# Optimization experiments

Measured on AMD Instinct MI355X. Metric: run time of the kernel, lower is better.

The kernel has to match this reference:

```python
import jax, jax.numpy as jnp
import numpy as np

B, S, D, DK = 4, 2048, 1024, 1024


def setup_inputs() -> dict:
    key = jax.random.key(0)
    kx, kq, kk, kv = jax.random.split(key, 4)
    return {
        "x": jax.random.normal(kx, (B, S, D), dtype=jnp.float32),
        "WQ": jax.random.normal(kq, (D, DK), dtype=jnp.float32),
        "WK": jax.random.normal(kk, (D, DK), dtype=jnp.float32),
        "WV": jax.random.normal(kv, (D, DK), dtype=jnp.float32),
    }


def reference(x, WQ, WK, WV):
    # q,k,v: [B,S,DK]
    q = x @ WQ
    k = x @ WK
    v = x @ WV
    scale = 1.0 / np.sqrt(DK).astype(np.float32)
    scores = jnp.einsum("bqd,bkd->bqk", q, k) * scale  # [B,S,S]
    # NOTE: original uses nn.Softmax(dim=1) -> normalize over the QUERY axis (axis 1)
    attn = jax.nn.softmax(scores, axis=1)
    return jnp.einsum("bqk,bkd->bqd", attn, v)
```

## Files before the change

### kernel.cpp

```cpp
#include <hip/hip_runtime.h>

constexpr int Bc  = 4;
constexpr int Sc  = 2048;
constexpr int Dc  = 1024;
constexpr int DKc = 1024;
constexpr long BSc = (long)Bc * Sc;

typedef __attribute__((ext_vector_type(8))) __bf16 bf16x8;
typedef __attribute__((ext_vector_type(4))) float  floatx4;

__device__ inline __bf16 f2bf(float f) {
  unsigned u = __builtin_bit_cast(unsigned, f);
  u = (u + 0x7FFFu + ((u >> 16) & 1u)) >> 16;
  unsigned short s = (unsigned short)u;
  return __builtin_bit_cast(__bf16, s);
}
__device__ inline float bf2f(__bf16 h) {
  unsigned u = ((unsigned)__builtin_bit_cast(unsigned short, h)) << 16;
  return __builtin_bit_cast(float, u);
}

__device__ inline void stage16(const __bf16* g, __bf16* l) {
  __builtin_amdgcn_global_load_lds(
      (const __attribute__((address_space(1))) unsigned int*)g,
      (__attribute__((address_space(3))) unsigned int*)l, 16, 0, 0);
}

__device__ __forceinline__ void bar_raw() {
  asm volatile("" ::: "memory");
  __builtin_amdgcn_s_barrier();
  asm volatile("" ::: "memory");
}
template <int N>
__device__ __forceinline__ void vmwait() {
  asm volatile("s_waitcnt vmcnt(%0)" :: "n"(N));
  __builtin_amdgcn_sched_barrier(0);
}

__global__ __launch_bounds__(256) void prep(
    const float* __restrict__ x,  __bf16* __restrict__ xhi, __bf16* __restrict__ xlo,
    const float* __restrict__ wq, __bf16* __restrict__ qhi, __bf16* __restrict__ qlo,
    const float* __restrict__ wk, __bf16* __restrict__ khi, __bf16* __restrict__ klo,
    const float* __restrict__ wv, __bf16* __restrict__ vthi) {
  __shared__ float tile[32][33];
  long blk = blockIdx.x;
  if (blk >= 40960) {
    int t   = (int)(blk - 40960);
    int bx  = t & 31, by = t >> 5;
    int thx = threadIdx.x & 31, thy = threadIdx.x >> 5;
    int xI  = bx * 32 + thx, yI = by * 32 + thy;
#pragma unroll
    for (int j = 0; j < 32; j += 8)
      tile[thy + j][thx] = wv[(long)(yI + j) * DKc + xI];
    __syncthreads();
    int xO = by * 32 + thx, yO = bx * 32 + thy;
#pragma unroll
    for (int j = 0; j < 32; j += 8)
      vthi[(long)(yO + j) * Dc + xO] = f2bf(tile[thx][thy + j]);
    return;
  }
  const float* in; __bf16 *hi, *lo; long base;
  if (blk < 32768)      { in = x;  hi = xhi; lo = xlo; base = blk * 256; }
  else if (blk < 36864) { in = wq; hi = qhi; lo = qlo; base = (blk - 32768) * 256; }
  else                  { in = wk; hi = khi; lo = klo; base = (blk - 36864) * 256; }
  long i = base + threadIdx.x;
  float f = in[i];
  __bf16 h = f2bf(f);
  hi[i] = h;
  lo[i] = f2bf(f - bf2f(h));
}

enum { MODE_QK = 0, MODE_V = 1, MODE_S = 2, MODE_PV = 3 };
constexpr int VSTR = 136;

template <int MODE>
__device__ __forceinline__ void gemm_body(
    char* smem,
    const __bf16* __restrict__ Ahi, const __bf16* __restrict__ Alo,
    const __bf16* __restrict__ Bhi, const __bf16* __restrict__ Blo,
    float* __restrict__ Cf, __bf16* __restrict__ Chi, __bf16* __restrict__ Clo,
    float* __restrict__ Pmax, float* __restrict__ Psum,
    const float* __restrict__ Ffac, float scale) {
  constexpr bool SPLIT = (MODE == MODE_QK || MODE == MODE_S);
  constexpr int  K = (MODE == MODE_PV) ? Sc : Dc;
  constexpr int  N = (MODE == MODE_S) ? Sc : DKc;
  constexpr long aBatch = (MODE == MODE_S) ? (long)Sc * DKc
                        : (MODE == MODE_PV) ? (long)Sc * Sc : 0;
  constexpr long bBatch = (MODE == MODE_S) ? (long)Sc * DKc
                        : (MODE == MODE_PV) ? (long)DKc * Sc : 0;
  constexpr long cBatch = (MODE == MODE_S) ? (long)Sc * Sc
                        : (MODE == MODE_PV) ? (long)Sc * DKc : 0;
  __bf16* sAh = (__bf16*)smem;
  __bf16* sBh = sAh + 128 * 32;
  __bf16* sAl = sBh + 128 * 32;
  __bf16* sBl = sAl + 128 * 32;

  const int b    = blockIdx.z;
  const int wave = threadIdx.x >> 6;
  const int lane = threadIdx.x & 63;
  const int wm   = wave >> 1;
  const int wn   = wave & 1;
  const int m0   = blockIdx.y * 128;
  const int n0   = blockIdx.x * 128;

  const __bf16* Ab  = Ahi + (long)b * aBatch + (long)m0 * K;
  const __bf16* Bb  = Bhi + (long)b * bBatch + (long)n0 * K;
  const __bf16* Abl = SPLIT ? Alo + (long)b * aBatch + (long)m0 * K : nullptr;
  const __bf16* Bbl = SPLIT ? Blo + (long)b * bBatch + (long)n0 * K : nullptr;
  const float*  Fb  = (MODE == MODE_PV)
                    ? Ffac + ((long)b * 8 + (blockIdx.y >> 1)) * Sc : nullptr;

  const int sr   = lane >> 2;
  const int sc_  = lane & 3;
  const int scol = (sc_ ^ ((sr >> 1) & 3)) * 8;

  floatx4 acc[4][4];
  const floatx4 zero = {0.f, 0.f, 0.f, 0.f};
#pragma unroll
  for (int i = 0; i < 4; ++i)
#pragma unroll
    for (int j = 0; j < 4; ++j) acc[i][j] = zero;

  const int frow = lane & 15;
  const int pko = ((lane >> 4) ^ ((frow >> 1) & 3)) * 8;

#pragma unroll 1
  for (int k0 = 0; k0 < K; k0 += 32) {
    if constexpr (MODE == MODE_PV) {
#pragma unroll
      for (int i = 0; i < 2; ++i) {
        const int rb = wave * 32 + i * 16;
        stage16(Bb + (long)(rb + sr) * K + k0 + scol, sBh + rb * 32);
      }
      const int tr = threadIdx.x >> 2;
      const int pc = threadIdx.x & 3;
#pragma unroll
      for (int h = 0; h < 2; ++h) {
        int r  = h * 64 + tr;
        int lc = pc ^ ((r >> 1) & 3);
        bf16x8 pv = *(const bf16x8*)(Ab + (long)r * K + k0 + lc * 8);
        const float* fp = Fb + k0 + lc * 8;
        bf16x8 o;
#pragma unroll
        for (int j = 0; j < 8; ++j) o[j] = f2bf(bf2f(pv[j]) * fp[j]);
        *(bf16x8*)(sAh + r * 32 + pc * 8) = o;
      }
    } else {
#pragma unroll
      for (int i = 0; i < 2; ++i) {
        const int rb = wave * 32 + i * 16;
        const long go = (long)(rb + sr) * K + k0 + scol;
        stage16(Ab + go, sAh + rb * 32);
        stage16(Bb + go, sBh + rb * 32);
        if constexpr (SPLIT) {
          stage16(Abl + go, sAl + rb * 32);
          stage16(Bbl + go, sBl + rb * 32);
        }
      }
    }
    __syncthreads();

    bf16x8 af[4], bfr[4], afl[4], bfl[4];
#pragma unroll
    for (int t = 0; t < 4; ++t) {
      af[t]  = *(const bf16x8*)(sAh + (wm * 64 + t * 16 + frow) * 32 + pko);
      bfr[t] = *(const bf16x8*)(sBh + (wn * 64 + t * 16 + frow) * 32 + pko);
      if constexpr (SPLIT) {
        afl[t] = *(const bf16x8*)(sAl + (wm * 64 + t * 16 + frow) * 32 + pko);
        bfl[t] = *(const bf16x8*)(sBl + (wn * 64 + t * 16 + frow) * 32 + pko);
      }
    }
#pragma unroll
    for (int mt = 0; mt < 4; ++mt)
#pragma unroll
      for (int nt = 0; nt < 4; ++nt) {
        acc[mt][nt] = __builtin_amdgcn_mfma_f32_16x16x32_bf16(af[mt], bfr[nt], acc[mt][nt], 0, 0, 0);
        if constexpr (SPLIT) {
          acc[mt][nt] = __builtin_amdgcn_mfma_f32_16x16x32_bf16(af[mt], bfl[nt], acc[mt][nt], 0, 0, 0);
          acc[mt][nt] = __builtin_amdgcn_mfma_f32_16x16x32_bf16(afl[mt], bfr[nt], acc[mt][nt], 0, 0, 0);
        }
      }
    __syncthreads();
  }

  const int crow0 = (lane >> 4) * 4;
  const int ccol  = lane & 15;
  const int tid   = threadIdx.x;

  if constexpr (MODE == MODE_V) {
    __bf16* sT = (__bf16*)smem;
#pragma unroll
    for (int nt = 0; nt < 4; ++nt) {
      int nl = wn * 64 + nt * 16 + ccol;
#pragma unroll
      for (int mt = 0; mt < 4; ++mt) {
        int ml = wm * 64 + mt * 16 + crow0;
#pragma unroll
        for (int r = 0; r < 4; ++r)
          sT[(long)nl * VSTR + ml + r] = f2bf(acc[mt][nt][r]);
      }
    }
    __syncthreads();
    const int bb   = m0 >> 11;
    const int seq0 = m0 & (Sc - 1);
    __bf16* dst = Chi + (long)bb * DKc * Sc + seq0;
#pragma unroll
    for (int c = 0; c < 8; ++c) {
      int flat = c * 2048 + tid * 8;
      int row = flat >> 7, col = flat & 127;
      *(bf16x8*)(dst + (long)(n0 + row) * Sc + col) =
          *(const bf16x8*)(sT + (long)row * VSTR + col);
    }
    return;
  }

  if constexpr (MODE == MODE_PV) {
#pragma unroll
    for (int nt = 0; nt < 4; ++nt) {
      int cn = n0 + wn * 64 + nt * 16 + ccol;
#pragma unroll
      for (int mt = 0; mt < 4; ++mt) {
#pragma unroll
        for (int r = 0; r < 4; ++r) {
          int cm_ = m0 + wm * 64 + mt * 16 + crow0 + r;
          Cf[(long)b * cBatch + (long)cm_ * N + cn] = acc[mt][nt][r] * scale;
        }
      }
    }
  }
}

__global__ __launch_bounds__(256) void gemm_v(
    const __bf16* __restrict__ xhi, const __bf16* __restrict__ wvthi,
    __bf16* __restrict__ vt) {
  __shared__ __align__(16) char smem[128 * VSTR * 2];
  gemm_body<MODE_V>(smem, xhi, nullptr, wvthi, nullptr, nullptr, vt, nullptr,
                    nullptr, nullptr, nullptr, 1.0f);
}

__global__ __launch_bounds__(256) void gemm_pv(
    const __bf16* __restrict__ P, const __bf16* __restrict__ vt,
    float* __restrict__ out, const float* __restrict__ ffac) {
  __shared__ __align__(16) char smem[16384];
  gemm_body<MODE_PV>(smem, P, nullptr, vt, nullptr, out, nullptr, nullptr,
                     nullptr, nullptr, ffac, 1.0f);
}

struct SCtx {
  const __bf16 *pAh, *pAl, *pBh, *pBl;
  __bf16* lds;
  int stLds;
  int aoff, boff;
};

template <int WA, int WB, int WC, bool SAL, bool S2A, bool S2B>
__device__ __forceinline__ void tile_step(const SCtx& c, int t,
                                          floatx4 (&acc)[8][4]) {
  constexpr int K = 1024;
  constexpr int BH = 8192, BL = 16384, AL = 24576;
  __bf16* cur = c.lds + (t & 1) * 32768;
  __bf16* oth = c.lds + ((t & 1) ^ 1) * 32768;
  bf16x8 af[8], bfr[4];

  vmwait<WA>();
  bar_raw();
#pragma unroll
  for (int mt = 0; mt < 8; ++mt)
    af[mt] = *(const bf16x8*)(cur + c.aoff + mt * 512);
#pragma unroll
  for (int nt = 0; nt < 4; ++nt)
    bfr[nt] = *(const bf16x8*)(cur + BH + c.boff + nt * 512);
  if (SAL) {
    const __bf16* s = c.pAl + (t + 1) * 32;
    stage16(s, oth + AL + c.stLds);
    stage16(s + 16 * K, oth + AL + c.stLds + 512);
  }
  bar_raw();
  __builtin_amdgcn_s_setprio(1);
#pragma unroll
  for (int mt = 0; mt < 8; ++mt)
#pragma unroll
    for (int nt = 0; nt < 4; ++nt)
      acc[mt][nt] = __builtin_amdgcn_mfma_f32_16x16x32_bf16(af[mt], bfr[nt], acc[mt][nt], 0, 0, 0);
  __builtin_amdgcn_s_setprio(0);

  vmwait<WB>();
  bar_raw();
  {
    bf16x8 bfl[4];
#pragma unroll
    for (int nt = 0; nt < 4; ++nt)
      bfl[nt] = *(const bf16x8*)(cur + BL + c.boff + nt * 512);
    if (S2A) {
      const __bf16* sa = c.pAh + (t + 2) * 32;
      stage16(sa, cur + c.stLds);
      stage16(sa + 16 * K, cur + c.stLds + 512);
      stage16(c.pBh + (t + 2) * 32, cur + BH + c.stLds);
    }
    bar_raw();
    __builtin_amdgcn_s_setprio(1);
#pragma unroll
    for (int mt = 0; mt < 8; ++mt)
#pragma unroll
      for (int nt = 0; nt < 4; ++nt)
        acc[mt][nt] = __builtin_amdgcn_mfma_f32_16x16x32_bf16(af[mt], bfl[nt], acc[mt][nt], 0, 0, 0);
    __builtin_amdgcn_s_setprio(0);
  }

  vmwait<WC>();
  bar_raw();
  {
    bf16x8 afl[8];
#pragma unroll
    for (int mt = 0; mt < 8; ++mt)
      afl[mt] = *(const bf16x8*)(cur + AL + c.aoff + mt * 512);
    if (S2B) {
      stage16(c.pBh + (t + 2) * 32 + 16 * K, cur + BH + c.stLds + 512);
      const __bf16* sb = c.pBl + (t + 2) * 32;
      stage16(sb, cur + BL + c.stLds);
      stage16(sb + 16 * K, cur + BL + c.stLds + 512);
    }
    bar_raw();
    __builtin_amdgcn_s_setprio(1);
#pragma unroll
    for (int mt = 0; mt < 8; ++mt)
#pragma unroll
      for (int nt = 0; nt < 4; ++nt)
        acc[mt][nt] = __builtin_amdgcn_mfma_f32_16x16x32_bf16(afl[mt], bfr[nt], acc[mt][nt], 0, 0, 0);
    __builtin_amdgcn_s_setprio(0);
  }
}

__global__ __launch_bounds__(512, 2) void gemm_s2(
    const __bf16* __restrict__ thi, const __bf16* __restrict__ tlo,
    const __bf16* __restrict__ xhi, const __bf16* __restrict__ xlo,
    __bf16* __restrict__ P, float* __restrict__ Pmax, float* __restrict__ Psum) {
  __shared__ __align__(16) __bf16 smem[65536];
  constexpr int K = 1024;
  const int b    = blockIdx.z;
  const int m0   = blockIdx.y * 256;
  const int n0   = blockIdx.x * 256;
  const int wave = threadIdx.x >> 6;
  const int lane = threadIdx.x & 63;
  const int wm   = wave >> 2;
  const int wn   = wave & 3;
  const int sr   = lane >> 2;
  const int scol = ((lane & 3) ^ ((sr >> 1) & 3)) * 8;
  const int frow = lane & 15;
  const int pko  = ((lane >> 4) ^ ((frow >> 1) & 3)) * 8;

  SCtx c;
  const long batch = (long)Sc * 1024;
  const long ar = (long)(m0 + wave * 32 + sr) * K + scol;
  const long br = (long)(n0 + wave * 32 + sr) * K + scol;
  c.pAh = thi + (long)b * batch + ar;
  c.pAl = tlo + (long)b * batch + ar;
  c.pBh = xhi + (long)b * batch + br;
  c.pBl = xlo + (long)b * batch + br;
  c.lds = smem;
  c.stLds = wave * 1024;
  c.aoff = (wm * 128 + frow) * 32 + pko;
  c.boff = (wn * 64 + frow) * 32 + pko;

  {
    __bf16* b0 = smem;
    __bf16* b1 = smem + 32768;
    stage16(c.pAh, b0 + c.stLds);               stage16(c.pAh + 16 * K, b0 + c.stLds + 512);
    stage16(c.pBh, b0 + 8192 + c.stLds);        stage16(c.pBh + 16 * K, b0 + 8192 + c.stLds + 512);
    stage16(c.pBl, b0 + 16384 + c.stLds);       stage16(c.pBl + 16 * K, b0 + 16384 + c.stLds + 512);
    stage16(c.pAl, b0 + 24576 + c.stLds);       stage16(c.pAl + 16 * K, b0 + 24576 + c.stLds + 512);
    stage16(c.pAh + 32, b1 + c.stLds);          stage16(c.pAh + 32 + 16 * K, b1 + c.stLds + 512);
    stage16(c.pBh + 32, b1 + 8192 + c.stLds);   stage16(c.pBh + 32 + 16 * K, b1 + 8192 + c.stLds + 512);
    stage16(c.pBl + 32, b1 + 16384 + c.stLds);  stage16(c.pBl + 32 + 16 * K, b1 + 16384 + c.stLds + 512);
  }

  floatx4 acc[8][4];
  const floatx4 zero = {0.f, 0.f, 0.f, 0.f};
#pragma unroll
  for (int i = 0; i < 8; ++i)
#pragma unroll
    for (int j = 0; j < 4; ++j) acc[i][j] = zero;

#pragma unroll 1
  for (int t = 0; t < 30; ++t) tile_step<10, 10, 11, true, true, true>(c, t, acc);
  tile_step<10, 10, 8, true, false, false>(c, 30, acc);
  tile_step<4, 2, 0, false, false, false>(c, 31, acc);

  const int crow0 = (lane >> 4) * 4;
  const int ccol  = lane & 15;
  const int tid   = threadIdx.x;
  constexpr float scale = 0.03125f;
  float* smax = (float*)smem;
  float* ssum = smax + 512;

  float cm[4];
#pragma unroll
  for (int nt = 0; nt < 4; ++nt) {
    float mx = -3.0e38f;
#pragma unroll
    for (int mt = 0; mt < 8; ++mt)
#pragma unroll
      for (int r = 0; r < 4; ++r) mx = fmaxf(mx, acc[mt][nt][r] * scale);
    cm[nt] = mx;
  }
#pragma unroll
  for (int off = 16; off <= 32; off <<= 1)
#pragma unroll
    for (int nt = 0; nt < 4; ++nt)
      cm[nt] = fmaxf(cm[nt], __shfl_xor(cm[nt], off, 64));
  __syncthreads();
  if (lane < 16)
#pragma unroll
    for (int nt = 0; nt < 4; ++nt)
      smax[wm * 256 + wn * 64 + nt * 16 + lane] = cm[nt];
  __syncthreads();
  float mfin[4];
#pragma unroll
  for (int nt = 0; nt < 4; ++nt) {
    int cidx = wn * 64 + nt * 16 + ccol;
    mfin[nt] = fmaxf(smax[cidx], smax[256 + cidx]);
  }
  float ps[4];
#pragma unroll
  for (int nt = 0; nt < 4; ++nt) {
    float s = 0.f;
#pragma unroll
    for (int mt = 0; mt < 8; ++mt)
#pragma unroll
      for (int r = 0; r < 4; ++r)
        s += __expf(acc[mt][nt][r] * scale - mfin[nt]);
    ps[nt] = s;
  }
#pragma unroll
  for (int off = 16; off <= 32; off <<= 1)
#pragma unroll
    for (int nt = 0; nt < 4; ++nt) ps[nt] += __shfl_xor(ps[nt], off, 64);
  if (lane < 16)
#pragma unroll
    for (int nt = 0; nt < 4; ++nt)
      ssum[wm * 256 + wn * 64 + nt * 16 + lane] = ps[nt];
  __syncthreads();
  if (tid < 256) {
    long o = ((long)b * 8 + blockIdx.y) * Sc + n0 + tid;
    Pmax[o] = fmaxf(smax[tid], smax[256 + tid]);
    Psum[o] = ssum[tid] + ssum[256 + tid];
  }
  __syncthreads();
  __bf16* sT = smem;
#pragma unroll
  for (int nt = 0; nt < 4; ++nt) {
    int col = wn * 64 + nt * 16 + ccol;
#pragma unroll
    for (int mt = 0; mt < 8; ++mt) {
      int rowb = wm * 128 + mt * 16 + crow0;
#pragma unroll
      for (int r = 0; r < 4; ++r) {
        int row = rowb + r;
        sT[row * 256 + (col ^ (((row >> 2) & 3) << 4))] =
            f2bf(__expf(acc[mt][nt][r] * scale - mfin[nt]));
      }
    }
  }
  __syncthreads();
  __bf16* Pb = P + (long)b * ((long)Sc * Sc);
#pragma unroll
  for (int cc = 0; cc < 16; ++cc) {
    int flat = cc * 4096 + tid * 8;
    int row = flat >> 8, col = flat & 255;
    *(bf16x8*)(Pb + (long)(m0 + row) * Sc + n0 + col) =
        *(const bf16x8*)(sT + row * 256 + (col ^ (((row >> 2) & 3) << 4)));
  }
}

struct TCtx {
  const __bf16 *pAh, *pAl, *pBh, *pBl;
  __bf16* lds;
  int stA, stB;
  int aoff, boff;
};

template <int WA, int WB, int WC, bool SAL, bool S2AB, bool S2B>
__device__ __forceinline__ void tile_step_t(const TCtx& c, int t,
                                            floatx4 (&acc)[4][4]) {
  constexpr int K = 1024;
  constexpr int BH = 8192, BL = 12288, AL = 16384, BUF = 24576;
  __bf16* cur = c.lds + (t & 1) * BUF;
  __bf16* oth = c.lds + ((t & 1) ^ 1) * BUF;
  bf16x8 af[4], bfr[4];

  vmwait<WA>();
  bar_raw();
#pragma unroll
  for (int mt = 0; mt < 4; ++mt)
    af[mt] = *(const bf16x8*)(cur + c.aoff + mt * 512);
#pragma unroll
  for (int nt = 0; nt < 4; ++nt)
    bfr[nt] = *(const bf16x8*)(cur + BH + c.boff + nt * 512);
  if (SAL) {
    const __bf16* s = c.pAl + (t + 1) * 32;
    stage16(s, oth + AL + c.stA);
    stage16(s + 16 * K, oth + AL + c.stA + 512);
  }
  bar_raw();
  __builtin_amdgcn_s_setprio(1);
#pragma unroll
  for (int mt = 0; mt < 4; ++mt)
#pragma unroll
    for (int nt = 0; nt < 4; ++nt)
      acc[mt][nt] = __builtin_amdgcn_mfma_f32_16x16x32_bf16(af[mt], bfr[nt], acc[mt][nt], 0, 0, 0);
  __builtin_amdgcn_s_setprio(0);

  vmwait<WB>();
  bar_raw();
  {
    bf16x8 bfl[4];
#pragma unroll
    for (int nt = 0; nt < 4; ++nt)
      bfl[nt] = *(const bf16x8*)(cur + BL + c.boff + nt * 512);
    if (S2AB) {
      const __bf16* sa = c.pAh + (t + 2) * 32;
      stage16(sa, cur + c.stA);
      stage16(sa + 16 * K, cur + c.stA + 512);
      stage16(c.pBh + (t + 2) * 32, cur + BH + c.stB);
    }
    bar_raw();
    __builtin_amdgcn_s_setprio(1);
#pragma unroll
    for (int mt = 0; mt < 4; ++mt)
#pragma unroll
      for (int nt = 0; nt < 4; ++nt)
        acc[mt][nt] = __builtin_amdgcn_mfma_f32_16x16x32_bf16(af[mt], bfl[nt], acc[mt][nt], 0, 0, 0);
    __builtin_amdgcn_s_setprio(0);
  }

  vmwait<WC>();
  bar_raw();
  {
    bf16x8 afl[4];
#pragma unroll
    for (int mt = 0; mt < 4; ++mt)
      afl[mt] = *(const bf16x8*)(cur + AL + c.aoff + mt * 512);
    if (S2B) stage16(c.pBl + (t + 2) * 32, cur + BL + c.stB);
    bar_raw();
    __builtin_amdgcn_s_setprio(1);
#pragma unroll
    for (int mt = 0; mt < 4; ++mt)
#pragma unroll
      for (int nt = 0; nt < 4; ++nt)
        acc[mt][nt] = __builtin_amdgcn_mfma_f32_16x16x32_bf16(afl[mt], bfr[nt], acc[mt][nt], 0, 0, 0);
    __builtin_amdgcn_s_setprio(0);
  }
}

__global__ __launch_bounds__(512, 2) void gemm_t2(
    const __bf16* __restrict__ xhi, const __bf16* __restrict__ xlo,
    const __bf16* __restrict__ gthi, const __bf16* __restrict__ gtlo,
    __bf16* __restrict__ thi, __bf16* __restrict__ tlo) {
  __shared__ __align__(16) __bf16 smem[49152];
  constexpr int K = 1024;
  const int m0   = blockIdx.y * 256;
  const int n0   = blockIdx.x * 128;
  const int wave = threadIdx.x >> 6;
  const int lane = threadIdx.x & 63;
  const int wm   = wave >> 1;
  const int wn   = wave & 1;
  const int sr   = lane >> 2;
  const int scol = ((lane & 3) ^ ((sr >> 1) & 3)) * 8;
  const int frow = lane & 15;
  const int pko  = ((lane >> 4) ^ ((frow >> 1) & 3)) * 8;

  TCtx c;
  const long ar = (long)(m0 + wave * 32 + sr) * K + scol;
  const long br = (long)(n0 + wave * 16 + sr) * K + scol;
  c.pAh = xhi + ar;
  c.pAl = xlo + ar;
  c.pBh = gthi + br;
  c.pBl = gtlo + br;
  c.lds = smem;
  c.stA = wave * 1024;
  c.stB = wave * 512;
  c.aoff = (wm * 64 + frow) * 32 + pko;
  c.boff = (wn * 64 + frow) * 32 + pko;

  {
    __bf16* b0 = smem;
    __bf16* b1 = smem + 24576;
    stage16(c.pAh, b0 + c.stA);          stage16(c.pAh + 16 * K, b0 + c.stA + 512);
    stage16(c.pBh, b0 + 8192 + c.stB);
    stage16(c.pBl, b0 + 12288 + c.stB);
    stage16(c.pAl, b0 + 16384 + c.stA);  stage16(c.pAl + 16 * K, b0 + 16384 + c.stA + 512);
    stage16(c.pAh + 32, b1 + c.stA);     stage16(c.pAh + 32 + 16 * K, b1 + c.stA + 512);
    stage16(c.pBh + 32, b1 + 8192 + c.stB);
    stage16(c.pBl + 32, b1 + 12288 + c.stB);
  }

  floatx4 acc[4][4];
  const floatx4 zero = {0.f, 0.f, 0.f, 0.f};
#pragma unroll
  for (int i = 0; i < 4; ++i)
#pragma unroll
    for (int j = 0; j < 4; ++j) acc[i][j] = zero;

#pragma unroll 1
  for (int t = 0; t < 30; ++t) tile_step_t<7, 8, 9, true, true, true>(c, t, acc);
  tile_step_t<7, 8, 6, true, false, false>(c, 30, acc);
  tile_step_t<3, 2, 0, false, false, false>(c, 31, acc);

  const int crow0 = (lane >> 4) * 4;
  const int ccol  = lane & 15;
  const int tid   = threadIdx.x;
  __bf16* sT = smem;
#pragma unroll 1
  for (int pass = 0; pass < 2; ++pass) {
    __syncthreads();
#pragma unroll
    for (int nt = 0; nt < 4; ++nt) {
      int col = wn * 64 + nt * 16 + ccol;
#pragma unroll
      for (int mt = 0; mt < 4; ++mt) {
        int rowb = wm * 64 + mt * 16 + crow0;
#pragma unroll
        for (int r = 0; r < 4; ++r) {
          int row = rowb + r;
          float v = acc[mt][nt][r];
          __bf16 h = f2bf(v);
          sT[row * 128 + (col ^ (((row >> 2) & 3) << 4))] =
              pass ? f2bf(v - bf2f(h)) : h;
        }
      }
    }
    __syncthreads();
    __bf16* dst = pass ? tlo : thi;
#pragma unroll
    for (int cc = 0; cc < 8; ++cc) {
      int flat = cc * 4096 + tid * 8;
      int row = flat >> 7, col = flat & 127;
      *(bf16x8*)(dst + (long)(m0 + row) * DKc + n0 + col) =
          *(const bf16x8*)(sT + row * 128 + (col ^ (((row >> 2) & 3) << 4)));
    }
  }
}

__global__ __launch_bounds__(256) void gemm_g64(
    const __bf16* __restrict__ Ahi, const __bf16* __restrict__ Alo,
    const __bf16* __restrict__ Bhi, const __bf16* __restrict__ Blo,
    __bf16* __restrict__ Chi, __bf16* __restrict__ Clo) {
  constexpr int K = Dc, N = DKc;
  __shared__ __align__(16) char smem[16384];
  __bf16* sAh = (__bf16*)smem;
  __bf16* sBh = sAh + 64 * 32;
  __bf16* sAl = sBh + 64 * 32;
  __bf16* sBl = sAl + 64 * 32;

  const int wave = threadIdx.x >> 6;
  const int lane = threadIdx.x & 63;
  const int wm   = wave >> 1, wn = wave & 1;
  const int m0   = blockIdx.y * 64;
  const int n0   = blockIdx.x * 64;

  const int sr   = lane >> 2;
  const int sc_  = lane & 3;
  const int scol = (sc_ ^ ((sr >> 1) & 3)) * 8;
  const int frow = lane & 15;
  const int pko  = ((lane >> 4) ^ ((frow >> 1) & 3)) * 8;

  floatx4 acc[2][2];
  const floatx4 zero = {0.f, 0.f, 0.f, 0.f};
#pragma unroll
  for (int i = 0; i < 2; ++i)
#pragma unroll
    for (int j = 0; j < 2; ++j) acc[i][j] = zero;

#pragma unroll 1
  for (int k0 = 0; k0 < K; k0 += 32) {
    const int rb = wave * 16;
    const long ga = (long)(m0 + rb + sr) * K + k0 + scol;
    const long gb = (long)(n0 + rb + sr) * K + k0 + scol;
    stage16(Ahi + ga, sAh + rb * 32);
    stage16(Alo + ga, sAl + rb * 32);
    stage16(Bhi + gb, sBh + rb * 32);
    stage16(Blo + gb, sBl + rb * 32);
    __syncthreads();

    bf16x8 af[2], bfr[2], afl[2], bfl[2];
#pragma unroll
    for (int t = 0; t < 2; ++t) {
      af[t]  = *(const bf16x8*)(sAh + (wm * 32 + t * 16 + frow) * 32 + pko);
      bfr[t] = *(const bf16x8*)(sBh + (wn * 32 + t * 16 + frow) * 32 + pko);
      afl[t] = *(const bf16x8*)(sAl + (wm * 32 + t * 16 + frow) * 32 + pko);
      bfl[t] = *(const bf16x8*)(sBl + (wn * 32 + t * 16 + frow) * 32 + pko);
    }
#pragma unroll
    for (int mt = 0; mt < 2; ++mt)
#pragma unroll
      for (int nt = 0; nt < 2; ++nt) {
        acc[mt][nt] = __builtin_amdgcn_mfma_f32_16x16x32_bf16(af[mt], bfr[nt], acc[mt][nt], 0, 0, 0);
        acc[mt][nt] = __builtin_amdgcn_mfma_f32_16x16x32_bf16(af[mt], bfl[nt], acc[mt][nt], 0, 0, 0);
        acc[mt][nt] = __builtin_amdgcn_mfma_f32_16x16x32_bf16(afl[mt], bfr[nt], acc[mt][nt], 0, 0, 0);
      }
    __syncthreads();
  }

  const int crow0 = (lane >> 4) * 4;
  const int ccol  = lane & 15;
  const int tid   = threadIdx.x;
  __bf16* sT = (__bf16*)smem;
#pragma unroll 1
  for (int pass = 0; pass < 2; ++pass) {
    __syncthreads();
#pragma unroll
    for (int nt = 0; nt < 2; ++nt) {
      int col = wn * 32 + nt * 16 + ccol;
#pragma unroll
      for (int mt = 0; mt < 2; ++mt) {
        int row = wm * 32 + mt * 16 + crow0;
#pragma unroll
        for (int r = 0; r < 4; ++r) {
          float v = acc[mt][nt][r];
          __bf16 h = f2bf(v);
          sT[(row + r) * 64 + col] = pass ? f2bf(v - bf2f(h)) : h;
        }
      }
    }
    __syncthreads();
    __bf16* dst = pass ? Clo : Chi;
#pragma unroll
    for (int c = 0; c < 2; ++c) {
      int flat = c * 2048 + tid * 8;
      int row = flat >> 6, col = flat & 63;
      *(bf16x8*)(dst + (long)(m0 + row) * N + n0 + col) = *(const bf16x8*)(sT + flat);
    }
  }
}

__global__ __launch_bounds__(256) void softmax_reduce(const float* __restrict__ Pmax,
                                                      const float* __restrict__ Psum,
                                                      float* __restrict__ Ffac) {
  int idx = blockIdx.x * 256 + threadIdx.x;
  int b = idx >> 11, k = idx & (Sc - 1);
  const float* pm = Pmax + (long)b * 8 * Sc + k;
  const float* ps = Psum + (long)b * 8 * Sc + k;
  float M = -3.0e38f;
#pragma unroll
  for (int t = 0; t < 8; ++t) M = fmaxf(M, pm[(long)t * Sc]);
  float S = 0.f;
#pragma unroll
  for (int t = 0; t < 8; ++t)
    S += ps[(long)t * Sc] * __expf(pm[(long)t * Sc] - M);
  float inv = 1.0f / S;
  float* fo = Ffac + (long)b * 8 * Sc + k;
#pragma unroll
  for (int t = 0; t < 8; ++t)
    fo[(long)t * Sc] = __expf(pm[(long)t * Sc] - M) * inv;
}

extern "C" void kernel_launch(void* const* d_in, const int* in_sizes, int n_in,
                              void* d_out, int out_size, void* d_ws, size_t ws_size,
                              hipStream_t stream) {
  const float* x  = (const float*)d_in[0];
  const float* WQ = (const float*)d_in[1];
  const float* WK = (const float*)d_in[2];
  const float* WV = (const float*)d_in[3];
  float* out = (float*)d_out;
  char* ws = (char*)d_ws;
  const long MB = 1024L * 1024L;

  __bf16* xhi  = (__bf16*)(ws + 0 * MB);
  __bf16* xlo  = (__bf16*)(ws + 16 * MB);
  __bf16* wqhi = (__bf16*)(ws + 32 * MB);
  __bf16* wqlo = (__bf16*)(ws + 34 * MB);
  __bf16* wkhi = (__bf16*)(ws + 36 * MB);
  __bf16* wklo = (__bf16*)(ws + 38 * MB);
  __bf16* wvthi= (__bf16*)(ws + 40 * MB);
  __bf16* gthi = (__bf16*)(ws + 44 * MB);
  __bf16* gtlo = (__bf16*)(ws + 46 * MB);
  __bf16* thi  = (__bf16*)(ws + 48 * MB);
  __bf16* tlo  = (__bf16*)(ws + 64 * MB);
  __bf16* vt   = (__bf16*)(ws + 80 * MB);
  __bf16* P    = (__bf16*)(ws + 96 * MB);
  float*  pmax = (float*)(ws + 128 * MB);
  float*  psum = (float*)(ws + 129 * MB);
  float*  ffac = (float*)(ws + 130 * MB);

  prep<<<41984, 256, 0, stream>>>(x, xhi, xlo, WQ, wqhi, wqlo, WK, wkhi, wklo,
                                  WV, wvthi);

  gemm_g64<<<dim3(16, 16), 256, 0, stream>>>(wkhi, wklo, wqhi, wqlo, gthi, gtlo);

  gemm_t2<<<dim3(DKc / 128, BSc / 256, 1), 512, 0, stream>>>(
      xhi, xlo, gthi, gtlo, thi, tlo);

  gemm_v<<<dim3(DKc / 128, BSc / 128, 1), 256, 0, stream>>>(xhi, wvthi, vt);

  gemm_s2<<<dim3(Sc / 256, Sc / 256, Bc), 512, 0, stream>>>(
      thi, tlo, xhi, xlo, P, pmax, psum);

  softmax_reduce<<<32, 256, 0, stream>>>(pmax, psum, ffac);

  gemm_pv<<<dim3(DKc / 128, Sc / 128, Bc), 256, 0, stream>>>(P, vt, out, ffac);
}
```

Before: 359.0 us.

## Split P scaling into separate pass and use triple-buffered async-staged PV GEMM

The softmax normalisation factor is now applied to P by a separate elementwise kernel instead of inside the PV GEMM's A-tile load. The PV GEMM is replaced by a 512-thread, 256x128-tile kernel that stages both operands straight into LDS with a three-deep buffer ring, waits on partial vmcnt and raises wave priority around the MFMAs. The goal is to overlap global loads with matrix math in the largest GEMM. The price is an extra full read and write of the P matrix, and more LDS per block, which may limit occupancy.

New measurement: 341.5 us. 4.9% less time.

```diff
diff --git a/kernel.cpp b/kernel.cpp
--- a/kernel.cpp
+++ b/kernel.cpp
@@ -70,32 +70,19 @@
   lo[i] = f2bf(f - bf2f(h));
 }
 
-enum { MODE_QK = 0, MODE_V = 1, MODE_S = 2, MODE_PV = 3 };
+enum { MODE_V = 1 };
 constexpr int VSTR = 136;
 
 template <int MODE>
 __device__ __forceinline__ void gemm_body(
     char* smem,
-    const __bf16* __restrict__ Ahi, const __bf16* __restrict__ Alo,
-    const __bf16* __restrict__ Bhi, const __bf16* __restrict__ Blo,
-    float* __restrict__ Cf, __bf16* __restrict__ Chi, __bf16* __restrict__ Clo,
-    float* __restrict__ Pmax, float* __restrict__ Psum,
-    const float* __restrict__ Ffac, float scale) {
-  constexpr bool SPLIT = (MODE == MODE_QK || MODE == MODE_S);
-  constexpr int  K = (MODE == MODE_PV) ? Sc : Dc;
-  constexpr int  N = (MODE == MODE_S) ? Sc : DKc;
-  constexpr long aBatch = (MODE == MODE_S) ? (long)Sc * DKc
-                        : (MODE == MODE_PV) ? (long)Sc * Sc : 0;
-  constexpr long bBatch = (MODE == MODE_S) ? (long)Sc * DKc
-                        : (MODE == MODE_PV) ? (long)DKc * Sc : 0;
-  constexpr long cBatch = (MODE == MODE_S) ? (long)Sc * Sc
-                        : (MODE == MODE_PV) ? (long)Sc * DKc : 0;
+    const __bf16* __restrict__ Ahi,
+    const __bf16* __restrict__ Bhi,
+    __bf16* __restrict__ Chi) {
+  constexpr int  K = Dc;
   __bf16* sAh = (__bf16*)smem;
   __bf16* sBh = sAh + 128 * 32;
-  __bf16* sAl = sBh + 128 * 32;
-  __bf16* sBl = sAl + 128 * 32;
-
-  const int b    = blockIdx.z;
+
   const int wave = threadIdx.x >> 6;
   const int lane = threadIdx.x & 63;
   const int wm   = wave >> 1;
@@ -103,12 +90,8 @@
   const int m0   = blockIdx.y * 128;
   const int n0   = blockIdx.x * 128;
 
-  const __bf16* Ab  = Ahi + (long)b * aBatch + (long)m0 * K;
-  const __bf16* Bb  = Bhi + (long)b * bBatch + (long)n0 * K;
-  const __bf16* Abl = SPLIT ? Alo + (long)b * aBatch + (long)m0 * K : nullptr;
-  const __bf16* Bbl = SPLIT ? Blo + (long)b * bBatch + (long)n0 * K : nullptr;
-  const float*  Fb  = (MODE == MODE_PV)
-                    ? Ffac + ((long)b * 8 + (blockIdx.y >> 1)) * Sc : nullptr;
+  const __bf16* Ab  = Ahi + (long)m0 * K;
+  const __bf16* Bb  = Bhi + (long)n0 * K;
 
   const int sr   = lane >> 2;
   const int sc_  = lane & 3;
@@ -126,60 +109,26 @@
 
 #pragma unroll 1
   for (int k0 = 0; k0 < K; k0 += 32) {
-    if constexpr (MODE == MODE_PV) {
-#pragma unroll
-      for (int i = 0; i < 2; ++i) {
-        const int rb = wave * 32 + i * 16;
-        stage16(Bb + (long)(rb + sr) * K + k0 + scol, sBh + rb * 32);
-      }
-      const int tr = threadIdx.x >> 2;
-      const int pc = threadIdx.x & 3;
-#pragma unroll
-      for (int h = 0; h < 2; ++h) {
-        int r  = h * 64 + tr;
-        int lc = pc ^ ((r >> 1) & 3);
-        bf16x8 pv = *(const bf16x8*)(Ab + (long)r * K + k0 + lc * 8);
-        const float* fp = Fb + k0 + lc * 8;
-        bf16x8 o;
-#pragma unroll
-        for (int j = 0; j < 8; ++j) o[j] = f2bf(bf2f(pv[j]) * fp[j]);
-        *(bf16x8*)(sAh + r * 32 + pc * 8) = o;
-      }
-    } else {
-#pragma unroll
-      for (int i = 0; i < 2; ++i) {
-        const int rb = wave * 32 + i * 16;
-        const long go = (long)(rb + sr) * K + k0 + scol;
-        stage16(Ab + go, sAh + rb * 32);
-        stage16(Bb + go, sBh + rb * 32);
-        if constexpr (SPLIT) {
-          stage16(Abl + go, sAl + rb * 32);
-          stage16(Bbl + go, sBl + rb * 32);
-        }
-      }
+#pragma unroll
+    for (int i = 0; i < 2; ++i) {
+      const int rb = wave * 32 + i * 16;
+      const long go = (long)(rb + sr) * K + k0 + scol;
+      stage16(Ab + go, sAh + rb * 32);
+      stage16(Bb + go, sBh + rb * 32);
     }
     __syncthreads();
 
-    bf16x8 af[4], bfr[4], afl[4], bfl[4];
+    bf16x8 af[4], bfr[4];
 #pragma unroll
     for (int t = 0; t < 4; ++t) {
       af[t]  = *(const bf16x8*)(sAh + (wm * 64 + t * 16 + frow) * 32 + pko);
       bfr[t] = *(const bf16x8*)(sBh + (wn * 64 + t * 16 + frow) * 32 + pko);
-      if constexpr (SPLIT) {
-        afl[t] = *(const bf16x8*)(sAl + (wm * 64 + t * 16 + frow) * 32 + pko);
-        bfl[t] = *(const bf16x8*)(sBl + (wn * 64 + t * 16 + frow) * 32 + pko);
-      }
     }
 #pragma unroll
     for (int mt = 0; mt < 4; ++mt)
 #pragma unroll
-      for (int nt = 0; nt < 4; ++nt) {
+      for (int nt = 0; nt < 4; ++nt)
         acc[mt][nt] = __builtin_amdgcn_mfma_f32_16x16x32_bf16(af[mt], bfr[nt], acc[mt][nt], 0, 0, 0);
-        if constexpr (SPLIT) {
-          acc[mt][nt] = __builtin_amdgcn_mfma_f32_16x16x32_bf16(af[mt], bfl[nt], acc[mt][nt], 0, 0, 0);
-          acc[mt][nt] = __builtin_amdgcn_mfma_f32_16x16x32_bf16(afl[mt], bfr[nt], acc[mt][nt], 0, 0, 0);
-        }
-      }
     __syncthreads();
   }
 
@@ -187,46 +136,28 @@
   const int ccol  = lane & 15;
   const int tid   = threadIdx.x;
 
-  if constexpr (MODE == MODE_V) {
-    __bf16* sT = (__bf16*)smem;
-#pragma unroll
-    for (int nt = 0; nt < 4; ++nt) {
-      int nl = wn * 64 + nt * 16 + ccol;
-#pragma unroll
-      for (int mt = 0; mt < 4; ++mt) {
-        int ml = wm * 64 + mt * 16 + crow0;
-#pragma unroll
-        for (int r = 0; r < 4; ++r)
-          sT[(long)nl * VSTR + ml + r] = f2bf(acc[mt][nt][r]);
-      }
-    }
-    __syncthreads();
-    const int bb   = m0 >> 11;
-    const int seq0 = m0 & (Sc - 1);
-    __bf16* dst = Chi + (long)bb * DKc * Sc + seq0;
-#pragma unroll
-    for (int c = 0; c < 8; ++c) {
-      int flat = c * 2048 + tid * 8;
-      int row = flat >> 7, col = flat & 127;
-      *(bf16x8*)(dst + (long)(n0 + row) * Sc + col) =
-          *(const bf16x8*)(sT + (long)row * VSTR + col);
-    }
-    return;
-  }
-
-  if constexpr (MODE == MODE_PV) {
-#pragma unroll
-    for (int nt = 0; nt < 4; ++nt) {
-      int cn = n0 + wn * 64 + nt * 16 + ccol;
-#pragma unroll
-      for (int mt = 0; mt < 4; ++mt) {
-#pragma unroll
-        for (int r = 0; r < 4; ++r) {
-          int cm_ = m0 + wm * 64 + mt * 16 + crow0 + r;
-          Cf[(long)b * cBatch + (long)cm_ * N + cn] = acc[mt][nt][r] * scale;
-        }
-      }
-    }
+  __bf16* sT = (__bf16*)smem;
+#pragma unroll
+  for (int nt = 0; nt < 4; ++nt) {
+    int nl = wn * 64 + nt * 16 + ccol;
+#pragma unroll
+    for (int mt = 0; mt < 4; ++mt) {
+      int ml = wm * 64 + mt * 16 + crow0;
+#pragma unroll
+      for (int r = 0; r < 4; ++r)
+        sT[(long)nl * VSTR + ml + r] = f2bf(acc[mt][nt][r]);
+    }
+  }
+  __syncthreads();
+  const int bb   = m0 >> 11;
+  const int seq0 = m0 & (Sc - 1);
+  __bf16* dst = Chi + (long)bb * DKc * Sc + seq0;
+#pragma unroll
+  for (int c = 0; c < 8; ++c) {
+    int flat = c * 2048 + tid * 8;
+    int row = flat >> 7, col = flat & 127;
+    *(bf16x8*)(dst + (long)(n0 + row) * Sc + col) =
+        *(const bf16x8*)(sT + (long)row * VSTR + col);
   }
 }
 
@@ -234,16 +165,7 @@
     const __bf16* __restrict__ xhi, const __bf16* __restrict__ wvthi,
     __bf16* __restrict__ vt) {
   __shared__ __align__(16) char smem[128 * VSTR * 2];
-  gemm_body<MODE_V>(smem, xhi, nullptr, wvthi, nullptr, nullptr, vt, nullptr,
-                    nullptr, nullptr, nullptr, 1.0f);
-}
-
-__global__ __launch_bounds__(256) void gemm_pv(
-    const __bf16* __restrict__ P, const __bf16* __restrict__ vt,
-    float* __restrict__ out, const float* __restrict__ ffac) {
-  __shared__ __align__(16) char smem[16384];
-  gemm_body<MODE_PV>(smem, P, nullptr, vt, nullptr, out, nullptr, nullptr,
-                     nullptr, nullptr, ffac, 1.0f);
+  gemm_body<MODE_V>(smem, xhi, wvthi, vt);
 }
 
 struct SCtx {
@@ -641,6 +563,163 @@
   }
 }
 
+__global__ __launch_bounds__(256) void scale_p(__bf16* __restrict__ P,
+                                               const float* __restrict__ ffac) {
+  long i8 = (long)blockIdx.x * 256 + threadIdx.x;
+  long base = i8 * 8;
+  int k = (int)(base & (Sc - 1));
+  int q = (int)((base >> 11) & (Sc - 1));
+  int b = (int)(base >> 22);
+  int t = q >> 8;
+  const float* f = ffac + (((long)b * 8 + t) << 11) + k;
+  float4 f0 = *(const float4*)f;
+  float4 f1 = *(const float4*)(f + 4);
+  bf16x8 p = *(const bf16x8*)(P + base);
+  bf16x8 o;
+  o[0] = f2bf(bf2f(p[0]) * f0.x);
+  o[1] = f2bf(bf2f(p[1]) * f0.y);
+  o[2] = f2bf(bf2f(p[2]) * f0.z);
+  o[3] = f2bf(bf2f(p[3]) * f0.w);
+  o[4] = f2bf(bf2f(p[4]) * f1.x);
+  o[5] = f2bf(bf2f(p[5]) * f1.y);
+  o[6] = f2bf(bf2f(p[6]) * f1.z);
+  o[7] = f2bf(bf2f(p[7]) * f1.w);
+  *(bf16x8*)(P + base) = o;
+}
+
+struct PCtx {
+  const __bf16 *pA, *pB;
+  int stA, stB;
+  int aoff, boff;
+};
+
+template <int WA, int WB, bool STG>
+__device__ __forceinline__ void tile_step_pv(const PCtx& c, int t,
+                                             __bf16* cur, __bf16* dst,
+                                             floatx4 (&acc)[4][4]) {
+  constexpr int K = 2048;
+  vmwait<WA>();
+  bar_raw();
+  {
+    bf16x8 af[4], bfr[4];
+#pragma unroll
+    for (int mt = 0; mt < 4; ++mt)
+      af[mt] = *(const bf16x8*)(cur + c.aoff + mt * 512);
+#pragma unroll
+    for (int nt = 0; nt < 4; ++nt)
+      bfr[nt] = *(const bf16x8*)(cur + 16384 + c.boff + nt * 512);
+    if (STG) {
+      const __bf16* a = c.pA + (t + 2) * 64;
+      stage16(a, dst + c.stA);
+      stage16(a + 16 * K, dst + c.stA + 512);
+      stage16(c.pB + (t + 2) * 64, dst + 16384 + c.stB);
+    }
+    bar_raw();
+    __builtin_amdgcn_s_setprio(1);
+#pragma unroll
+    for (int mt = 0; mt < 4; ++mt)
+#pragma unroll
+      for (int nt = 0; nt < 4; ++nt)
+        acc[mt][nt] = __builtin_amdgcn_mfma_f32_16x16x32_bf16(af[mt], bfr[nt], acc[mt][nt], 0, 0, 0);
+    __builtin_amdgcn_s_setprio(0);
+  }
+  vmwait<WB>();
+  bar_raw();
+  {
+    bf16x8 af[4], bfr[4];
+#pragma unroll
+    for (int mt = 0; mt < 4; ++mt)
+      af[mt] = *(const bf16x8*)(cur + 8192 + c.aoff + mt * 512);
+#pragma unroll
+    for (int nt = 0; nt < 4; ++nt)
+      bfr[nt] = *(const bf16x8*)(cur + 20480 + c.boff + nt * 512);
+    if (STG) {
+      const __bf16* a = c.pA + (t + 2) * 64 + 32;
+      stage16(a, dst + 8192 + c.stA);
+      stage16(a + 16 * K, dst + 8192 + c.stA + 512);
+      stage16(c.pB + (t + 2) * 64 + 32, dst + 20480 + c.stB);
+    }
+    bar_raw();
+    __builtin_amdgcn_s_setprio(1);
+#pragma unroll
+    for (int mt = 0; mt < 4; ++mt)
+#pragma unroll
+      for (int nt = 0; nt < 4; ++nt)
+        acc[mt][nt] = __builtin_amdgcn_mfma_f32_16x16x32_bf16(af[mt], bfr[nt], acc[mt][nt], 0, 0, 0);
+    __builtin_amdgcn_s_setprio(0);
+  }
+}
+
+__global__ __launch_bounds__(512, 2) void gemm_pv2(
+    const __bf16* __restrict__ P, const __bf16* __restrict__ vt,
+    float* __restrict__ out) {
+  __shared__ __align__(16) __bf16 smem[73728];
+  constexpr int K = 2048;
+  const int b    = blockIdx.z;
+  const int m0   = blockIdx.x * 256;
+  const int n0   = blockIdx.y * 128;
+  const int wave = threadIdx.x >> 6;
+  const int lane = threadIdx.x & 63;
+  const int wm   = wave >> 1;
+  const int wn   = wave & 1;
+  const int sr   = lane >> 2;
+  const int scol = ((lane & 3) ^ ((sr >> 1) & 3)) * 8;
+  const int frow = lane & 15;
+  const int pko  = ((lane >> 4) ^ ((frow >> 1) & 3)) * 8;
+
+  PCtx c;
+  c.pA = P + (long)b * Sc * Sc + (long)(m0 + wave * 32 + sr) * K + scol;
+  c.pB = vt + (long)b * DKc * Sc + (long)(n0 + wave * 16 + sr) * K + scol;
+  c.stA = wave * 1024;
+  c.stB = wave * 512;
+  c.aoff = (wm * 64 + frow) * 32 + pko;
+  c.boff = (wn * 64 + frow) * 32 + pko;
+
+  __bf16* B0 = smem;
+  __bf16* B1 = smem + 24576;
+  __bf16* B2 = smem + 49152;
+
+  stage16(c.pA, B0 + c.stA);            stage16(c.pA + 16 * K, B0 + c.stA + 512);
+  stage16(c.pB, B0 + 16384 + c.stB);
+  stage16(c.pA + 32, B0 + 8192 + c.stA); stage16(c.pA + 32 + 16 * K, B0 + 8192 + c.stA + 512);
+  stage16(c.pB + 32, B0 + 20480 + c.stB);
+  stage16(c.pA + 64, B1 + c.stA);       stage16(c.pA + 64 + 16 * K, B1 + c.stA + 512);
+  stage16(c.pB + 64, B1 + 16384 + c.stB);
+  stage16(c.pA + 96, B1 + 8192 + c.stA); stage16(c.pA + 96 + 16 * K, B1 + 8192 + c.stA + 512);
+  stage16(c.pB + 96, B1 + 20480 + c.stB);
+
+  floatx4 acc[4][4];
+  const floatx4 zero = {0.f, 0.f, 0.f, 0.f};
+#pragma unroll
+  for (int i = 0; i < 4; ++i)
+#pragma unroll
+    for (int j = 0; j < 4; ++j) acc[i][j] = zero;
+
+#pragma unroll 1
+  for (int t = 0; t < 30; t += 3) {
+    tile_step_pv<9, 9, true>(c, t,     B0, B2, acc);
+    tile_step_pv<9, 9, true>(c, t + 1, B1, B0, acc);
+    tile_step_pv<9, 9, true>(c, t + 2, B2, B1, acc);
+  }
+  tile_step_pv<9, 6, false>(c, 30, B0, B0, acc);
+  tile_step_pv<3, 0, false>(c, 31, B1, B1, acc);
+
+  const int crow0 = (lane >> 4) * 4;
+  const int ccol  = lane & 15;
+#pragma unroll
+  for (int nt = 0; nt < 4; ++nt) {
+    int cn = n0 + wn * 64 + nt * 16 + ccol;
+#pragma unroll
+    for (int mt = 0; mt < 4; ++mt) {
+#pragma unroll
+      for (int r = 0; r < 4; ++r) {
+        int cm_ = m0 + wm * 64 + mt * 16 + crow0 + r;
+        out[(long)b * Sc * DKc + (long)cm_ * DKc + cn] = acc[mt][nt][r];
+      }
+    }
+  }
+}
+
 __global__ __launch_bounds__(256) void gemm_g64(
     const __bf16* __restrict__ Ahi, const __bf16* __restrict__ Alo,
     const __bf16* __restrict__ Bhi, const __bf16* __restrict__ Blo,
@@ -797,5 +876,7 @@
 
   softmax_reduce<<<32, 256, 0, stream>>>(pmax, psum, ffac);
 
-  gemm_pv<<<dim3(DKc / 128, Sc / 128, Bc), 256, 0, stream>>>(P, vt, out, ffac);
-}
+  scale_p<<<8192, 256, 0, stream>>>(P, ffac);
+
+  gemm_pv2<<<dim3(Sc / 256, DKc / 128, Bc), 512, 0, stream>>>(P, vt, out);
+}
```
